# Kernel optimization log

Hardware: AMD Instinct MI355X
Metric: run time of the kernel (lower is better)

The kernel has to match this reference:

```python
import jax, jax.numpy as jnp
import numpy as np

B, N, I, H = 4, 325, 64, 128
LN_EPS = 1e-5

def setup_inputs() -> dict:
    key = jax.random.key(0)
    ks = jax.random.split(key, 20)
    x = jax.random.normal(ks[0], (B, N, I), dtype=jnp.float32)
    # sparse binary adjacency with self-loops (as the module masks adj == 0)
    a = (jax.random.uniform(ks[1], (B, N, N)) < 0.05).astype(jnp.float32)
    adj = jnp.maximum(a, jnp.eye(N, dtype=jnp.float32)[None])
    h = jax.random.normal(ks[2], (B, N, H), dtype=jnp.float32)
    c = jax.random.normal(ks[3], (B, N, H), dtype=jnp.float32)
    def glorot(k, shape):
        fan_in, fan_out = shape[-1], shape[0]
        s = jnp.sqrt(2.0 / (fan_in + fan_out)).astype(jnp.float32)
        return jax.random.normal(k, shape, dtype=jnp.float32) * s
    params = {
        'W_ih': glorot(ks[4], (4 * H, I)),
        'W_hh': glorot(ks[5], (4 * H, H)),
        'b_ih': jnp.zeros((4 * H,), jnp.float32),
        'b_hh': jnp.zeros((4 * H,), jnp.float32),
        'gc_w': glorot(ks[6], (H, H)),
        'gc_b': jnp.zeros((H,), jnp.float32),
        'Ws_w': glorot(ks[7], (H, H)),
        'Ws_b': jnp.zeros((H,), jnp.float32),
        'Wt_w': glorot(ks[8], (H, H)),
        'Wt_b': jnp.zeros((H,), jnp.float32),
        'v': glorot(ks[9], (H, 1)),
        'ln_g': jnp.ones((H,), jnp.float32),
        'ln_b': jnp.zeros((H,), jnp.float32),
        'comb_w': glorot(ks[10], (H, 2 * H)),
        'comb_b': jnp.zeros((H,), jnp.float32),
    }
    return {'x': x, 'adj': adj, 'h': h, 'c': c, **params}


def reference(x, adj, h, c, W_ih, W_hh, b_ih, b_hh, gc_w, gc_b,
              Ws_w, Ws_b, Wt_w, Wt_b, v, ln_g, ln_b, comb_w, comb_b):
    # --- LSTMCell applied per node (PyTorch gate order: i, f, g, o) ---
    gates = (jnp.einsum('bni,gi->bng', x, W_ih) + b_ih
             + jnp.einsum('bnh,gh->bng', h, W_hh) + b_hh)  # [B,N,4H]
    i_g, f_g, g_g, o_g = jnp.split(gates, 4, axis=-1)
    c_lstm = jax.nn.sigmoid(f_g) * c + jax.nn.sigmoid(i_g) * jnp.tanh(g_g)
    h_lstm = jax.nn.sigmoid(o_g) * jnp.tanh(c_lstm)  # [B,N,H]
    # --- Graph convolution: adj @ (h W) + b ---
    support = jnp.einsum('bnh,ho->bno', h_lstm, gc_w)
    h_graph = jnp.einsum('bnm,bmo->bno', adj, support) + gc_b
    # --- Spatial attention (tanh-additive, adjacency-masked softmax) ---
    s = jnp.einsum('bnh,oh->bno', h_graph, Ws_w) + Ws_b  # W_s(x)
    t = jnp.einsum('bnh,oh->bno', h_graph, Wt_w) + Wt_b  # W_t(x)
    # scores[b,i,j] = tanh(s[b,i] + t[b,j]) @ v ; big [B,N,N,H] intermediate
    scores = jnp.einsum('bijh,h->bij',
                        jnp.tanh(s[:, :, None, :] + t[:, None, :, :]),
                        v[:, 0])
    scores = jnp.where(adj == 0, -1e9, scores)
    attn = jax.nn.softmax(scores, axis=-1)
    context = jnp.einsum('bij,bjh->bih', attn, h_graph)
    # --- LayerNorm ---
    mu = jnp.mean(context, axis=-1, keepdims=True)
    var = jnp.var(context, axis=-1, keepdims=True)
    h_att = ln_g * (context - mu) * jax.lax.rsqrt(var + LN_EPS) + ln_b
    # --- Combine ---
    h_comb = jnp.concatenate([h_lstm, h_att], axis=-1)
    h_new = jnp.einsum('bnk,ok->bno', h_comb, comb_w) + comb_b
    return (h_new, c_lstm)
```

## Files before the change

### kernel.cpp

```cpp
#include <hip/hip_runtime.h>

#define B_ 4
#define N_ 325
#define I_ 64
#define H_ 128
#define NODES (B_ * N_)
#define NZMAX 64
#define NBLK (NODES / 4)

typedef unsigned short u16;
typedef unsigned int u32;

__device__ __align__(16) float g_WT   [192 * 512];
__device__ __align__(16) float g_gcw  [128 * 128];
__device__ __align__(16) float g_WsT  [128 * 128];
__device__ __align__(16) float g_WtT  [128 * 128];
__device__ __align__(16) float g_combT[256 * 128];
__device__ float g_bias[512];
__device__ float g_svec[896];

__device__ __align__(16) float g_support[(size_t)NODES * H_];
__device__ __align__(16) float g_h_graph[(size_t)NODES * H_];
__device__ __align__(16) float g_s_buf  [(size_t)NODES * H_];
__device__ __align__(16) float g_t_buf  [(size_t)NODES * H_];
__device__ __align__(16) float g_hl     [(size_t)NODES * H_];
__device__ u16 g_nz [(size_t)NODES * NZMAX];
__device__ int g_nzc[NODES];

__device__ __forceinline__ float bf2f(u16 u) { return __uint_as_float(((u32)u) << 16); }
__device__ __forceinline__ u16 f2bf(float f) {
    u32 u = __float_as_uint(f);
    u += 0x7fffu + ((u >> 16) & 1u);
    return (u16)(u >> 16);
}
__device__ __forceinline__ float ldin(const void* p, size_t i, int f32) {
    return f32 ? ((const float*)p)[i] : bf2f(((const u16*)p)[i]);
}
__device__ __forceinline__ void stout(void* p, size_t i, float v, int f32) {
    if (f32) ((float*)p)[i] = v; else ((u16*)p)[i] = f2bf(v);
}
__device__ __forceinline__ float fast_rcp(float x) { return __builtin_amdgcn_rcpf(x); }
__device__ __forceinline__ float sigm(float x) { return fast_rcp(1.f + __expf(-x)); }
__device__ __forceinline__ float tanh_f(float x) {
    x = fminf(15.f, fmaxf(-15.f, x));
    float e = __expf(2.f * x);
    return (e - 1.f) * fast_rcp(e + 1.f);
}
__device__ __forceinline__ int probe_f32(const void* adj) {
    return ((((const u32*)adj)[0] & 0xFFFFu) != 0x3F80u) ? 1 : 0;
}

__global__ __launch_bounds__(256) void k0_prep(
    const void* __restrict__ W_ih, const void* __restrict__ W_hh,
    const void* __restrict__ b_ih, const void* __restrict__ b_hh,
    const void* __restrict__ gc_w, const void* __restrict__ gc_b,
    const void* __restrict__ Ws_w, const void* __restrict__ Ws_b,
    const void* __restrict__ Wt_w, const void* __restrict__ Wt_b,
    const void* __restrict__ vvec, const void* __restrict__ ln_g,
    const void* __restrict__ ln_b, const void* __restrict__ comb_w,
    const void* __restrict__ comb_b, const void* __restrict__ adj)
{
    const int f32 = probe_f32(adj);
    const int tid = blockIdx.x * 256 + threadIdx.x;
    const int nth = gridDim.x * 256;
    const int TOT = 98304 + 16384 * 3 + 32768 + 512 + 896;
    for (int e = tid; e < TOT; e += nth) {
        int i = e;
        if (i < 98304) {
            const int k = i >> 9, g = i & 511;
            g_WT[i] = (k < 64) ? ldin(W_ih, (size_t)g * 64 + k, f32)
                               : ldin(W_hh, (size_t)g * 128 + (k - 64), f32);
            continue;
        }
        i -= 98304;
        if (i < 16384) { g_gcw[i] = ldin(gc_w, i, f32); continue; }
        i -= 16384;
        if (i < 16384) {
            const int k = i >> 7, o = i & 127;
            g_WsT[i] = ldin(Ws_w, (size_t)o * 128 + k, f32);
            continue;
        }
        i -= 16384;
        if (i < 16384) {
            const int k = i >> 7, o = i & 127;
            g_WtT[i] = ldin(Wt_w, (size_t)o * 128 + k, f32);
            continue;
        }
        i -= 16384;
        if (i < 32768) {
            const int k = i >> 7, o = i & 127;
            g_combT[i] = ldin(comb_w, (size_t)o * 256 + k, f32);
            continue;
        }
        i -= 32768;
        if (i < 512) { g_bias[i] = ldin(b_ih, i, f32) + ldin(b_hh, i, f32); continue; }
        i -= 512;
        {
            const int seg = i >> 7, k = i & 127;
            const void* src = (seg == 0) ? gc_b : (seg == 1) ? Ws_b : (seg == 2) ? Wt_b :
                              (seg == 3) ? vvec : (seg == 4) ? ln_g : (seg == 5) ? ln_b : comb_b;
            g_svec[i] = ldin(src, k, f32);
        }
    }
}

__global__ __launch_bounds__(512) void k1_lstm(
    const void* __restrict__ x, const void* __restrict__ h, const void* __restrict__ c,
    const void* __restrict__ adj, void* __restrict__ out)
{
    const int f32 = probe_f32(adj);
    __shared__ __align__(16) float4 xh4[192];
    __shared__ __align__(16) float4 Gt4[512];
    __shared__ __align__(16) float4 hl4[128];
    const int node0 = blockIdx.x * 4;
    const int t = threadIdx.x;

    for (int e = t; e < 768; e += 512) {
        const int n = e / 192, k = e % 192;
        const int node = node0 + n;
        ((float*)&xh4[k])[n] = (k < 64) ? ldin(x, (size_t)node * 64 + k, f32)
                                        : ldin(h, (size_t)node * 128 + (k - 64), f32);
    }
    __syncthreads();

    {
        const int g = t;
        float a0 = 0.f, a1 = 0.f, a2 = 0.f, a3 = 0.f;
        #pragma unroll 8
        for (int k = 0; k < 192; ++k) {
            const float wv = g_WT[(size_t)k * 512 + g];
            const float4 xv = xh4[k];
            a0 = fmaf(xv.x, wv, a0); a1 = fmaf(xv.y, wv, a1);
            a2 = fmaf(xv.z, wv, a2); a3 = fmaf(xv.w, wv, a3);
        }
        const float bias = g_bias[g];
        Gt4[g] = make_float4(a0 + bias, a1 + bias, a2 + bias, a3 + bias);
    }
    __syncthreads();

    {
        const int n = t >> 7, hh = t & 127;
        const int node = node0 + n;
        float ig = ((const float*)&Gt4[hh])[n];
        float fg = ((const float*)&Gt4[128 + hh])[n];
        float gv = ((const float*)&Gt4[256 + hh])[n];
        float og = ((const float*)&Gt4[384 + hh])[n];
        float cl = sigm(fg) * ldin(c, (size_t)node * 128 + hh, f32) + sigm(ig) * tanh_f(gv);
        float hv = sigm(og) * tanh_f(cl);
        stout(out, (size_t)(NODES * H_) + (size_t)node * 128 + hh, cl, f32);
        g_hl[(size_t)node * 128 + hh] = hv;
        ((float*)&hl4[hh])[n] = hv;
    }
    __syncthreads();

    {
        const int o = t & 127, n = t >> 7;
        float acc = 0.f;
        #pragma unroll 8
        for (int k = 0; k < 128; ++k)
            acc = fmaf(((const float*)&hl4[k])[n], g_gcw[(size_t)k * 128 + o], acc);
        g_support[(size_t)(node0 + n) * 128 + o] = acc;
    }
}

__global__ __launch_bounds__(256) void k2_graph(const void* __restrict__ adj)
{
    const int f32 = probe_f32(adj);
    __shared__ __align__(16) float4 hg4[128];
    __shared__ u16 nzi[4][NZMAX];
    __shared__ float nzv[4][NZMAX];
    __shared__ int cnt[4];
    const int node0 = blockIdx.x * 4;
    const int t = threadIdx.x;
    const int lane = t & 63, w = t >> 6;

    if (t < 4) cnt[t] = 0;
    __syncthreads();
    for (int j = lane; j < N_; j += 64) {
        float a = ldin(adj, (size_t)(node0 + w) * N_ + j, f32);
        if (a != 0.f) {
            int p = atomicAdd(&cnt[w], 1);
            if (p < NZMAX) { nzi[w][p] = (u16)j; nzv[w][p] = a; }
        }
    }
    __syncthreads();
    if (t < 4) g_nzc[node0 + t] = min(cnt[t], NZMAX);
    #pragma unroll
    for (int n = 0; n < 4; ++n) {
        const int cnn = min(cnt[n], NZMAX);
        for (int p = t; p < cnn; p += 256) g_nz[(size_t)(node0 + n) * NZMAX + p] = nzi[n][p];
    }

    const int o = t & 127;
    const float gb = g_svec[o];
    #pragma unroll
    for (int ps = 0; ps < 2; ++ps) {
        const int n = (t >> 7) + 2 * ps;
        const int node = node0 + n;
        const int bn = node / N_;
        const int cnn = min(cnt[n], NZMAX);
        float acc = gb;
        for (int p = 0; p < cnn; ++p)
            acc = fmaf(nzv[n][p], g_support[((size_t)bn * N_ + nzi[n][p]) * 128 + o], acc);
        g_h_graph[(size_t)node * 128 + o] = acc;
        ((float*)&hg4[o])[n] = acc;
    }
    __syncthreads();

    {
        const int which = t >> 7;
        const float* WT = which ? g_WtT : g_WsT;
        const float bias = g_svec[128 + which * 128 + o];
        float a0 = 0.f, a1 = 0.f, a2 = 0.f, a3 = 0.f;
        #pragma unroll 8
        for (int k = 0; k < 128; ++k) {
            const float wv = WT[(size_t)k * 128 + o];
            const float4 hv = hg4[k];
            a0 = fmaf(hv.x, wv, a0); a1 = fmaf(hv.y, wv, a1);
            a2 = fmaf(hv.z, wv, a2); a3 = fmaf(hv.w, wv, a3);
        }
        float* dst = which ? g_t_buf : g_s_buf;
        dst[(size_t)(node0 + 0) * 128 + o] = a0 + bias;
        dst[(size_t)(node0 + 1) * 128 + o] = a1 + bias;
        dst[(size_t)(node0 + 2) * 128 + o] = a2 + bias;
        dst[(size_t)(node0 + 3) * 128 + o] = a3 + bias;
    }
}

__global__ __launch_bounds__(256) void k3_attn(
    const void* __restrict__ adj, void* __restrict__ out)
{
    const int f32 = probe_f32(adj);
    __shared__ __align__(16) float4 comb4[256];
    __shared__ float s_i[4][H_];
    __shared__ float red[4][H_];
    __shared__ float nzs[4][NZMAX];
    __shared__ u16 nzi[4][NZMAX];
    __shared__ float part[2][4][H_];
    __shared__ float mu_[4], rstd_[4], smv[4];
    __shared__ int cnt[4];
    const int node0 = blockIdx.x * 4;
    const int t = threadIdx.x;
    const int lane = t & 63, w = t >> 6;

    if (t < 4) cnt[t] = g_nzc[node0 + t];
    for (int e = t; e < 512; e += 256) {
        const int n = e >> 7, k = e & 127;
        const int node = node0 + n;
        s_i[n][k] = g_s_buf[(size_t)node * 128 + k];
        ((float*)&comb4[k])[n] = g_hl[(size_t)node * 128 + k];
    }
    __syncthreads();
    #pragma unroll
    for (int n = 0; n < 4; ++n)
        for (int p = t; p < cnt[n]; p += 256) nzi[n][p] = g_nz[(size_t)(node0 + n) * NZMAX + p];
    __syncthreads();

    {
        const int bn = (node0 + w) / N_;
        const int cn = cnt[w];
        const float v0 = g_svec[384 + lane], v1 = g_svec[384 + 64 + lane];
        const float si0 = s_i[w][lane], si1 = s_i[w][lane + 64];
        for (int p = 0; p < cn; ++p) {
            const float* tj = g_t_buf + ((size_t)bn * N_ + nzi[w][p]) * 128;
            float a = v0 * tanh_f(si0 + tj[lane]) + v1 * tanh_f(si1 + tj[lane + 64]);
            #pragma unroll
            for (int off = 32; off > 0; off >>= 1) a += __shfl_xor(a, off);
            if (lane == 0) nzs[w][p] = a;
        }
    }
    __syncthreads();

    if (t < 4) {
        const int cn = cnt[t];
        float m = -1e30f;
        for (int p = 0; p < cn; ++p) m = fmaxf(m, nzs[t][p]);
        float ssum = 0.f;
        for (int p = 0; p < cn; ++p) { float e = __expf(nzs[t][p] - m); nzs[t][p] = e; ssum += e; }
        smv[t] = fast_rcp(ssum);
    }
    __syncthreads();

    const int o = t & 127;
    #pragma unroll
    for (int ps = 0; ps < 2; ++ps) {
        const int n = (t >> 7) + 2 * ps;
        const int bn = (node0 + n) / N_;
        const int cn = cnt[n];
        float acc = 0.f;
        for (int p = 0; p < cn; ++p)
            acc = fmaf(nzs[n][p], g_h_graph[((size_t)bn * N_ + nzi[n][p]) * 128 + o], acc);
        red[n][o] = acc * smv[n];
    }
    __syncthreads();

    {
        float x0 = red[w][lane], x1 = red[w][lane + 64];
        float sm = x0 + x1, sq = x0 * x0 + x1 * x1;
        #pragma unroll
        for (int off = 32; off > 0; off >>= 1) {
            sm += __shfl_xor(sm, off);
            sq += __shfl_xor(sq, off);
        }
        if (lane == 0) {
            float mu = sm * (1.f / H_);
            float var = fmaxf(sq * (1.f / H_) - mu * mu, 0.f);
            mu_[w] = mu;
            rstd_[w] = __builtin_amdgcn_rsqf(var + 1e-5f);
        }
    }
    __syncthreads();
    for (int e = t; e < 512; e += 256) {
        const int n = e >> 7, k = e & 127;
        float xn = (red[n][k] - mu_[n]) * rstd_[n];
        ((float*)&comb4[128 + k])[n] = g_svec[512 + k] * xn + g_svec[640 + k];
    }
    __syncthreads();

    {
        const int half = t >> 7;
        float a0 = 0.f, a1 = 0.f, a2 = 0.f, a3 = 0.f;
        const int k0 = half * 128;
        #pragma unroll 8
        for (int kk = 0; kk < 128; ++kk) {
            const int k = k0 + kk;
            const float wv = g_combT[(size_t)k * 128 + o];
            const float4 cv = comb4[k];
            a0 = fmaf(cv.x, wv, a0); a1 = fmaf(cv.y, wv, a1);
            a2 = fmaf(cv.z, wv, a2); a3 = fmaf(cv.w, wv, a3);
        }
        part[half][0][o] = a0; part[half][1][o] = a1;
        part[half][2][o] = a2; part[half][3][o] = a3;
    }
    __syncthreads();
    for (int e = t; e < 512; e += 256) {
        const int n = e >> 7, k = e & 127;
        stout(out, (size_t)(node0 + n) * 128 + k,
              part[0][n][k] + part[1][n][k] + g_svec[768 + k], f32);
    }
}

extern "C" void kernel_launch(void* const* d_in, const int* in_sizes, int n_in,
                              void* d_out, int out_size, void* d_ws, size_t ws_size,
                              hipStream_t stream)
{
    (void)in_sizes; (void)n_in; (void)out_size; (void)d_ws; (void)ws_size;
    const void* x      = d_in[0];
    const void* adj    = d_in[1];
    const void* h      = d_in[2];
    const void* c      = d_in[3];
    const void* W_ih   = d_in[4];
    const void* W_hh   = d_in[5];
    const void* b_ih   = d_in[6];
    const void* b_hh   = d_in[7];
    const void* gc_w   = d_in[8];
    const void* gc_b   = d_in[9];
    const void* Ws_w   = d_in[10];
    const void* Ws_b   = d_in[11];
    const void* Wt_w   = d_in[12];
    const void* Wt_b   = d_in[13];
    const void* vvec   = d_in[14];
    const void* ln_g   = d_in[15];
    const void* ln_b   = d_in[16];
    const void* comb_w = d_in[17];
    const void* comb_b = d_in[18];

    k0_prep <<<256, 256, 0, stream>>>(W_ih, W_hh, b_ih, b_hh, gc_w, gc_b,
                                      Ws_w, Ws_b, Wt_w, Wt_b, vvec, ln_g, ln_b,
                                      comb_w, comb_b, adj);
    k1_lstm <<<NBLK, 512, 0, stream>>>(x, h, c, adj, d_out);
    k2_graph<<<NBLK, 256, 0, stream>>>(adj);
    k3_attn <<<NBLK, 256, 0, stream>>>(adj, d_out);
}
```

Baseline: 152.2 us.

## Fuse prep, LSTM, graph and attention kernels into one cooperative kernel

```diff
diff --git a/kernel.cpp b/kernel.cpp
--- a/kernel.cpp
+++ b/kernel.cpp
@@ -1,4 +1,7 @@
 #include <hip/hip_runtime.h>
+#include <hip/hip_cooperative_groups.h>
+
+namespace cg = cooperative_groups;
 
 #define B_ 4
 #define N_ 325
@@ -21,8 +24,8 @@
 
 __device__ __align__(16) float g_support[(size_t)NODES * H_];
 __device__ __align__(16) float g_h_graph[(size_t)NODES * H_];
+__device__ __align__(16) float g_t_buf  [(size_t)NODES * H_];
 __device__ __align__(16) float g_s_buf  [(size_t)NODES * H_];
-__device__ __align__(16) float g_t_buf  [(size_t)NODES * H_];
 __device__ __align__(16) float g_hl     [(size_t)NODES * H_];
 __device__ u16 g_nz [(size_t)NODES * NZMAX];
 __device__ int g_nzc[NODES];
@@ -48,6 +51,273 @@
 }
 __device__ __forceinline__ int probe_f32(const void* adj) {
     return ((((const u32*)adj)[0] & 0xFFFFu) != 0x3F80u) ? 1 : 0;
+}
+
+#define PREP_TOT (98304 + 16384 * 3 + 32768 + 512 + 896)
+
+__device__ __forceinline__ void prep_elem(int e, int f32,
+    const void* W_ih, const void* W_hh, const void* b_ih, const void* b_hh,
+    const void* gc_w, const void* gc_b, const void* Ws_w, const void* Ws_b,
+    const void* Wt_w, const void* Wt_b, const void* vvec, const void* ln_g,
+    const void* ln_b, const void* comb_w, const void* comb_b)
+{
+    int i = e;
+    if (i < 98304) {
+        const int k = i >> 9, g = i & 511;
+        g_WT[i] = (k < 64) ? ldin(W_ih, (size_t)g * 64 + k, f32)
+                           : ldin(W_hh, (size_t)g * 128 + (k - 64), f32);
+        return;
+    }
+    i -= 98304;
+    if (i < 16384) { g_gcw[i] = ldin(gc_w, i, f32); return; }
+    i -= 16384;
+    if (i < 16384) {
+        const int k = i >> 7, o = i & 127;
+        g_WsT[i] = ldin(Ws_w, (size_t)o * 128 + k, f32);
+        return;
+    }
+    i -= 16384;
+    if (i < 16384) {
+        const int k = i >> 7, o = i & 127;
+        g_WtT[i] = ldin(Wt_w, (size_t)o * 128 + k, f32);
+        return;
+    }
+    i -= 16384;
+    if (i < 32768) {
+        const int k = i >> 7, o = i & 127;
+        g_combT[i] = ldin(comb_w, (size_t)o * 256 + k, f32);
+        return;
+    }
+    i -= 32768;
+    if (i < 512) { g_bias[i] = ldin(b_ih, i, f32) + ldin(b_hh, i, f32); return; }
+    i -= 512;
+    {
+        const int seg = i >> 7, k = i & 127;
+        const void* src = (seg == 0) ? gc_b : (seg == 1) ? Ws_b : (seg == 2) ? Wt_b :
+                          (seg == 3) ? vvec : (seg == 4) ? ln_g : (seg == 5) ? ln_b : comb_b;
+        g_svec[i] = ldin(src, k, f32);
+    }
+}
+
+__global__ __launch_bounds__(512, 4) void k_fused(
+    const void* __restrict__ x, const void* __restrict__ adj,
+    const void* __restrict__ h, const void* __restrict__ c,
+    const void* __restrict__ W_ih, const void* __restrict__ W_hh,
+    const void* __restrict__ b_ih, const void* __restrict__ b_hh,
+    const void* __restrict__ gc_w, const void* __restrict__ gc_b,
+    const void* __restrict__ Ws_w, const void* __restrict__ Ws_b,
+    const void* __restrict__ Wt_w, const void* __restrict__ Wt_b,
+    const void* __restrict__ vvec, const void* __restrict__ ln_g,
+    const void* __restrict__ ln_b, const void* __restrict__ comb_w,
+    const void* __restrict__ comb_b, void* __restrict__ out)
+{
+    cg::grid_group grid = cg::this_grid();
+    const int f32 = probe_f32(adj);
+    const int t = threadIdx.x;
+    const int node0 = blockIdx.x * 4;
+    const int lane = t & 63, w = t >> 6;
+
+    __shared__ __align__(16) float4 xh4[192];
+    __shared__ __align__(16) float4 Gt4[512];
+    __shared__ __align__(16) float4 hl4[128];
+    __shared__ __align__(16) float4 hg4[128];
+    __shared__ __align__(16) float4 att4[128];
+    __shared__ u16 nzi[4][NZMAX];
+    __shared__ float nzv[4][NZMAX];
+    __shared__ float nzs[4][NZMAX];
+    __shared__ int cnt[4];
+    __shared__ float s_i[4][H_];
+    __shared__ float red[4][H_];
+    __shared__ float part[4][4][H_];
+    __shared__ float mu_[4], rstd_[4], smv[4];
+
+    {
+        const int tid = blockIdx.x * 512 + t;
+        const int nth = gridDim.x * 512;
+        for (int e = tid; e < PREP_TOT; e += nth)
+            prep_elem(e, f32, W_ih, W_hh, b_ih, b_hh, gc_w, gc_b, Ws_w, Ws_b,
+                      Wt_w, Wt_b, vvec, ln_g, ln_b, comb_w, comb_b);
+    }
+    grid.sync();
+
+    for (int e = t; e < 768; e += 512) {
+        const int n = e / 192, k = e % 192;
+        const int node = node0 + n;
+        ((float*)&xh4[k])[n] = (k < 64) ? ldin(x, (size_t)node * 64 + k, f32)
+                                        : ldin(h, (size_t)node * 128 + (k - 64), f32);
+    }
+    __syncthreads();
+    {
+        const int g = t;
+        float a0 = 0.f, a1 = 0.f, a2 = 0.f, a3 = 0.f;
+        #pragma unroll 8
+        for (int k = 0; k < 192; ++k) {
+            const float wv = g_WT[(size_t)k * 512 + g];
+            const float4 xv = xh4[k];
+            a0 = fmaf(xv.x, wv, a0); a1 = fmaf(xv.y, wv, a1);
+            a2 = fmaf(xv.z, wv, a2); a3 = fmaf(xv.w, wv, a3);
+        }
+        const float bias = g_bias[g];
+        Gt4[g] = make_float4(a0 + bias, a1 + bias, a2 + bias, a3 + bias);
+    }
+    __syncthreads();
+    {
+        const int n = t >> 7, hh = t & 127;
+        const int node = node0 + n;
+        float ig = ((const float*)&Gt4[hh])[n];
+        float fg = ((const float*)&Gt4[128 + hh])[n];
+        float gv = ((const float*)&Gt4[256 + hh])[n];
+        float og = ((const float*)&Gt4[384 + hh])[n];
+        float cl = sigm(fg) * ldin(c, (size_t)node * 128 + hh, f32) + sigm(ig) * tanh_f(gv);
+        float hv = sigm(og) * tanh_f(cl);
+        stout(out, (size_t)(NODES * H_) + (size_t)node * 128 + hh, cl, f32);
+        ((float*)&hl4[hh])[n] = hv;
+    }
+    __syncthreads();
+    {
+        const int o = t & 127, n = t >> 7;
+        float acc = 0.f;
+        #pragma unroll 8
+        for (int k = 0; k < 128; ++k)
+            acc = fmaf(((const float*)&hl4[k])[n], g_gcw[(size_t)k * 128 + o], acc);
+        g_support[(size_t)(node0 + n) * 128 + o] = acc;
+    }
+    grid.sync();
+
+    if (t < 4) cnt[t] = 0;
+    __syncthreads();
+    {
+        const int n = t >> 7, jj = t & 127;
+        const size_t row = (size_t)(node0 + n) * N_;
+        for (int j = jj; j < N_; j += 128) {
+            float a = ldin(adj, row + j, f32);
+            if (a != 0.f) {
+                int p = atomicAdd(&cnt[n], 1);
+                if (p < NZMAX) { nzi[n][p] = (u16)j; nzv[n][p] = a; }
+            }
+        }
+    }
+    __syncthreads();
+    {
+        const int n = t >> 7, o = t & 127;
+        const int node = node0 + n;
+        const int bn = node / N_;
+        const int cn = min(cnt[n], NZMAX);
+        float acc = g_svec[o];
+        for (int p = 0; p < cn; ++p)
+            acc = fmaf(nzv[n][p], g_support[((size_t)bn * N_ + nzi[n][p]) * 128 + o], acc);
+        g_h_graph[(size_t)node * 128 + o] = acc;
+        ((float*)&hg4[o])[n] = acc;
+    }
+    __syncthreads();
+    {
+        const int o = t & 127;
+        const int which = (t >> 7) & 1;
+        const int half  = t >> 8;
+        const float* WT = which ? g_WtT : g_WsT;
+        const int k0 = half * 64;
+        float a0 = 0.f, a1 = 0.f, a2 = 0.f, a3 = 0.f;
+        #pragma unroll 8
+        for (int kk = 0; kk < 64; ++kk) {
+            const int k = k0 + kk;
+            const float wv = WT[(size_t)k * 128 + o];
+            const float4 hv = hg4[k];
+            a0 = fmaf(hv.x, wv, a0); a1 = fmaf(hv.y, wv, a1);
+            a2 = fmaf(hv.z, wv, a2); a3 = fmaf(hv.w, wv, a3);
+        }
+        const int s = which * 2 + half;
+        part[s][0][o] = a0; part[s][1][o] = a1;
+        part[s][2][o] = a2; part[s][3][o] = a3;
+    }
+    __syncthreads();
+    for (int e = t; e < 1024; e += 512) {
+        const int which = e >> 9, n = (e >> 7) & 3, o = e & 127;
+        const float vsum = part[which * 2][n][o] + part[which * 2 + 1][n][o]
+                         + g_svec[128 + which * 128 + o];
+        if (which) g_t_buf[(size_t)(node0 + n) * 128 + o] = vsum;
+        else       s_i[n][o] = vsum;
+    }
+    grid.sync();
+
+    {
+        const int n = w & 3;
+        const int bn = (node0 + n) / N_;
+        const int cn = min(cnt[n], NZMAX);
+        const float v0 = g_svec[384 + lane], v1 = g_svec[384 + 64 + lane];
+        const float si0 = s_i[n][lane], si1 = s_i[n][lane + 64];
+        for (int p = (w >> 2); p < cn; p += 2) {
+            const float* tj = g_t_buf + ((size_t)bn * N_ + nzi[n][p]) * 128;
+            float a = v0 * tanh_f(si0 + tj[lane]) + v1 * tanh_f(si1 + tj[lane + 64]);
+            #pragma unroll
+            for (int off = 32; off > 0; off >>= 1) a += __shfl_xor(a, off);
+            if (lane == 0) nzs[n][p] = a;
+        }
+    }
+    __syncthreads();
+    if (t < 4) {
+        const int cn = min(cnt[t], NZMAX);
+        float m = -1e30f;
+        for (int p = 0; p < cn; ++p) m = fmaxf(m, nzs[t][p]);
+        float ssum = 0.f;
+        for (int p = 0; p < cn; ++p) { float e = __expf(nzs[t][p] - m); nzs[t][p] = e; ssum += e; }
+        smv[t] = fast_rcp(ssum);
+    }
+    __syncthreads();
+    {
+        const int n = t >> 7, o = t & 127;
+        const int bn = (node0 + n) / N_;
+        const int cn = min(cnt[n], NZMAX);
+        float acc = 0.f;
+        for (int p = 0; p < cn; ++p)
+            acc = fmaf(nzs[n][p], g_h_graph[((size_t)bn * N_ + nzi[n][p]) * 128 + o], acc);
+        red[n][o] = acc * smv[n];
+    }
+    __syncthreads();
+    if (w < 4) {
+        float x0 = red[w][lane], x1 = red[w][lane + 64];
+        float sm = x0 + x1, sq = x0 * x0 + x1 * x1;
+        #pragma unroll
+        for (int off = 32; off > 0; off >>= 1) {
+            sm += __shfl_xor(sm, off);
+            sq += __shfl_xor(sq, off);
+        }
+        if (lane == 0) {
+            float mu = sm * (1.f / H_);
+            float var = fmaxf(sq * (1.f / H_) - mu * mu, 0.f);
+            mu_[w] = mu;
+            rstd_[w] = __builtin_amdgcn_rsqf(var + 1e-5f);
+        }
+    }
+    __syncthreads();
+    {
+        const int n = t >> 7, k = t & 127;
+        float xn = (red[n][k] - mu_[n]) * rstd_[n];
+        ((float*)&att4[k])[n] = g_svec[512 + k] * xn + g_svec[640 + k];
+    }
+    __syncthreads();
+    {
+        const int o = t & 127, q = t >> 7;
+        const float4* src = (q < 2) ? hl4 : att4;
+        const int kb = (q < 2) ? q * 64 : (q - 2) * 64;
+        const int k0 = q * 64;
+        float a0 = 0.f, a1 = 0.f, a2 = 0.f, a3 = 0.f;
+        #pragma unroll 8
+        for (int kk = 0; kk < 64; ++kk) {
+            const float wv = g_combT[(size_t)(k0 + kk) * 128 + o];
+            const float4 cv = src[kb + kk];
+            a0 = fmaf(cv.x, wv, a0); a1 = fmaf(cv.y, wv, a1);
+            a2 = fmaf(cv.z, wv, a2); a3 = fmaf(cv.w, wv, a3);
+        }
+        part[q][0][o] = a0; part[q][1][o] = a1;
+        part[q][2][o] = a2; part[q][3][o] = a3;
+    }
+    __syncthreads();
+    {
+        const int n = t >> 7, k = t & 127;
+        stout(out, (size_t)(node0 + n) * 128 + k,
+              part[0][n][k] + part[1][n][k] + part[2][n][k] + part[3][n][k]
+              + g_svec[768 + k], f32);
+    }
 }
 
 __global__ __launch_bounds__(256) void k0_prep(
@@ -63,45 +333,9 @@
     const int f32 = probe_f32(adj);
     const int tid = blockIdx.x * 256 + threadIdx.x;
     const int nth = gridDim.x * 256;
-    const int TOT = 98304 + 16384 * 3 + 32768 + 512 + 896;
-    for (int e = tid; e < TOT; e += nth) {
-        int i = e;
-        if (i < 98304) {
-            const int k = i >> 9, g = i & 511;
-            g_WT[i] = (k < 64) ? ldin(W_ih, (size_t)g * 64 + k, f32)
-                               : ldin(W_hh, (size_t)g * 128 + (k - 64), f32);
-            continue;
-        }
-        i -= 98304;
-        if (i < 16384) { g_gcw[i] = ldin(gc_w, i, f32); continue; }
-        i -= 16384;
-        if (i < 16384) {
-            const int k = i >> 7, o = i & 127;
-            g_WsT[i] = ldin(Ws_w, (size_t)o * 128 + k, f32);
-            continue;
-        }
-        i -= 16384;
-        if (i < 16384) {
-            const int k = i >> 7, o = i & 127;
-            g_WtT[i] = ldin(Wt_w, (size_t)o * 128 + k, f32);
-            continue;
-        }
-        i -= 16384;
-        if (i < 32768) {
-            const int k = i >> 7, o = i & 127;
-            g_combT[i] = ldin(comb_w, (size_t)o * 256 + k, f32);
-            continue;
-        }
-        i -= 32768;
-        if (i < 512) { g_bias[i] = ldin(b_ih, i, f32) + ldin(b_hh, i, f32); continue; }
-        i -= 512;
-        {
-            const int seg = i >> 7, k = i & 127;
-            const void* src = (seg == 0) ? gc_b : (seg == 1) ? Ws_b : (seg == 2) ? Wt_b :
-                              (seg == 3) ? vvec : (seg == 4) ? ln_g : (seg == 5) ? ln_b : comb_b;
-            g_svec[i] = ldin(src, k, f32);
-        }
-    }
+    for (int e = tid; e < PREP_TOT; e += nth)
+        prep_elem(e, f32, W_ih, W_hh, b_ih, b_hh, gc_w, gc_b, Ws_w, Ws_b,
+                  Wt_w, Wt_b, vvec, ln_g, ln_b, comb_w, comb_b);
 }
 
 __global__ __launch_bounds__(512) void k1_lstm(
@@ -122,7 +356,6 @@
                                         : ldin(h, (size_t)node * 128 + (k - 64), f32);
     }
     __syncthreads();
-
     {
         const int g = t;
         float a0 = 0.f, a1 = 0.f, a2 = 0.f, a3 = 0.f;
@@ -137,7 +370,6 @@
         Gt4[g] = make_float4(a0 + bias, a1 + bias, a2 + bias, a3 + bias);
     }
     __syncthreads();
-
     {
         const int n = t >> 7, hh = t & 127;
         const int node = node0 + n;
@@ -152,7 +384,6 @@
         ((float*)&hl4[hh])[n] = hv;
     }
     __syncthreads();
-
     {
         const int o = t & 127, n = t >> 7;
         float acc = 0.f;
@@ -206,7 +437,6 @@
         ((float*)&hg4[o])[n] = acc;
     }
     __syncthreads();
-
     {
         const int which = t >> 7;
         const float* WT = which ? g_WtT : g_WsT;
@@ -270,7 +500,6 @@
         }
     }
     __syncthreads();
-
     if (t < 4) {
         const int cn = cnt[t];
         float m = -1e30f;
@@ -280,7 +509,6 @@
         smv[t] = fast_rcp(ssum);
     }
     __syncthreads();
-
     const int o = t & 127;
     #pragma unroll
     for (int ps = 0; ps < 2; ++ps) {
@@ -293,7 +521,6 @@
         red[n][o] = acc * smv[n];
     }
     __syncthreads();
-
     {
         float x0 = red[w][lane], x1 = red[w][lane + 64];
         float sm = x0 + x1, sq = x0 * x0 + x1 * x1;
@@ -316,7 +543,6 @@
         ((float*)&comb4[128 + k])[n] = g_svec[512 + k] * xn + g_svec[640 + k];
     }
     __syncthreads();
-
     {
         const int half = t >> 7;
         float a0 = 0.f, a1 = 0.f, a2 = 0.f, a3 = 0.f;
@@ -365,10 +591,22 @@
     const void* comb_w = d_in[17];
     const void* comb_b = d_in[18];
 
-    k0_prep <<<256, 256, 0, stream>>>(W_ih, W_hh, b_ih, b_hh, gc_w, gc_b,
-                                      Ws_w, Ws_b, Wt_w, Wt_b, vvec, ln_g, ln_b,
-                                      comb_w, comb_b, adj);
-    k1_lstm <<<NBLK, 512, 0, stream>>>(x, h, c, adj, d_out);
-    k2_graph<<<NBLK, 256, 0, stream>>>(adj);
-    k3_attn <<<NBLK, 256, 0, stream>>>(adj, d_out);
-}
+    void* args[] = {
+        (void*)&x, (void*)&adj, (void*)&h, (void*)&c,
+        (void*)&W_ih, (void*)&W_hh, (void*)&b_ih, (void*)&b_hh,
+        (void*)&gc_w, (void*)&gc_b, (void*)&Ws_w, (void*)&Ws_b,
+        (void*)&Wt_w, (void*)&Wt_b, (void*)&vvec, (void*)&ln_g,
+        (void*)&ln_b, (void*)&comb_w, (void*)&comb_b, (void*)&d_out
+    };
+    hipError_t err = hipLaunchCooperativeKernel(
+        reinterpret_cast<void*>(k_fused), dim3(NBLK), dim3(512),
+        args, 0, stream);
+    if (err != hipSuccess) {
+        k0_prep <<<256, 256, 0, stream>>>(W_ih, W_hh, b_ih, b_hh, gc_w, gc_b,
+                                          Ws_w, Ws_b, Wt_w, Wt_b, vvec, ln_g, ln_b,
+                                          comb_w, comb_b, adj);
+        k1_lstm <<<NBLK, 512, 0, stream>>>(x, h, c, adj, d_out);
+        k2_graph<<<NBLK, 256, 0, stream>>>(adj);
+        k3_attn <<<NBLK, 256, 0, stream>>>(adj, d_out);
+    }
+}
```

Result: slower. 276.7 us (+81.9%).

## Drop weight-prep kernel, read raw weights directly, move adjacency compaction into LSTM kernel

Applied to the files above, without the earlier changes.

```diff
diff --git a/kernel.cpp b/kernel.cpp
--- a/kernel.cpp
+++ b/kernel.cpp
@@ -11,21 +11,14 @@
 typedef unsigned short u16;
 typedef unsigned int u32;
 
-__device__ __align__(16) float g_WT   [192 * 512];
-__device__ __align__(16) float g_gcw  [128 * 128];
-__device__ __align__(16) float g_WsT  [128 * 128];
-__device__ __align__(16) float g_WtT  [128 * 128];
-__device__ __align__(16) float g_combT[256 * 128];
-__device__ float g_bias[512];
-__device__ float g_svec[896];
-
 __device__ __align__(16) float g_support[(size_t)NODES * H_];
 __device__ __align__(16) float g_h_graph[(size_t)NODES * H_];
+__device__ __align__(16) float g_t_buf  [(size_t)NODES * H_];
 __device__ __align__(16) float g_s_buf  [(size_t)NODES * H_];
-__device__ __align__(16) float g_t_buf  [(size_t)NODES * H_];
 __device__ __align__(16) float g_hl     [(size_t)NODES * H_];
-__device__ u16 g_nz [(size_t)NODES * NZMAX];
-__device__ int g_nzc[NODES];
+__device__ u16   g_nz [(size_t)NODES * NZMAX];
+__device__ float g_nzw[(size_t)NODES * NZMAX];
+__device__ int   g_nzc[NODES];
 
 __device__ __forceinline__ float bf2f(u16 u) { return __uint_as_float(((u32)u) << 16); }
 __device__ __forceinline__ u16 f2bf(float f) {
@@ -33,11 +26,19 @@
     u += 0x7fffu + ((u >> 16) & 1u);
     return (u16)(u >> 16);
 }
-__device__ __forceinline__ float ldin(const void* p, size_t i, int f32) {
-    return f32 ? ((const float*)p)[i] : bf2f(((const u16*)p)[i]);
-}
-__device__ __forceinline__ void stout(void* p, size_t i, float v, int f32) {
-    if (f32) ((float*)p)[i] = v; else ((u16*)p)[i] = f2bf(v);
+template<int F32>
+__device__ __forceinline__ float ldw(const void* p, size_t i) {
+    return F32 ? ((const float*)p)[i] : bf2f(((const u16*)p)[i]);
+}
+template<int F32>
+__device__ __forceinline__ float4 ldw4(const void* p, size_t i4) {
+    if (F32) return ((const float4*)p)[i4];
+    const ushort4 u = ((const ushort4*)p)[i4];
+    return make_float4(bf2f(u.x), bf2f(u.y), bf2f(u.z), bf2f(u.w));
+}
+template<int F32>
+__device__ __forceinline__ void stw(void* p, size_t i, float v) {
+    if (F32) ((float*)p)[i] = v; else ((u16*)p)[i] = f2bf(v);
 }
 __device__ __forceinline__ float fast_rcp(float x) { return __builtin_amdgcn_rcpf(x); }
 __device__ __forceinline__ float sigm(float x) { return fast_rcp(1.f + __expf(-x)); }
@@ -50,174 +51,180 @@
     return ((((const u32*)adj)[0] & 0xFFFFu) != 0x3F80u) ? 1 : 0;
 }
 
-__global__ __launch_bounds__(256) void k0_prep(
+struct LdsA {
+    float4 xh4[192];
+    float4 Gt4[512];
+    float4 hl4[128];
+    u16 nzi[4][NZMAX];
+    float nzv[4][NZMAX];
+    int cnt[4];
+};
+
+template<int F32>
+__device__ __forceinline__ void d1_body(LdsA& S,
+    const void* __restrict__ x, const void* __restrict__ adjp,
+    const void* __restrict__ h, const void* __restrict__ c,
     const void* __restrict__ W_ih, const void* __restrict__ W_hh,
     const void* __restrict__ b_ih, const void* __restrict__ b_hh,
-    const void* __restrict__ gc_w, const void* __restrict__ gc_b,
-    const void* __restrict__ Ws_w, const void* __restrict__ Ws_b,
-    const void* __restrict__ Wt_w, const void* __restrict__ Wt_b,
-    const void* __restrict__ vvec, const void* __restrict__ ln_g,
-    const void* __restrict__ ln_b, const void* __restrict__ comb_w,
-    const void* __restrict__ comb_b, const void* __restrict__ adj)
-{
-    const int f32 = probe_f32(adj);
-    const int tid = blockIdx.x * 256 + threadIdx.x;
-    const int nth = gridDim.x * 256;
-    const int TOT = 98304 + 16384 * 3 + 32768 + 512 + 896;
-    for (int e = tid; e < TOT; e += nth) {
-        int i = e;
-        if (i < 98304) {
-            const int k = i >> 9, g = i & 511;
-            g_WT[i] = (k < 64) ? ldin(W_ih, (size_t)g * 64 + k, f32)
-                               : ldin(W_hh, (size_t)g * 128 + (k - 64), f32);
-            continue;
-        }
-        i -= 98304;
-        if (i < 16384) { g_gcw[i] = ldin(gc_w, i, f32); continue; }
-        i -= 16384;
-        if (i < 16384) {
-            const int k = i >> 7, o = i & 127;
-            g_WsT[i] = ldin(Ws_w, (size_t)o * 128 + k, f32);
-            continue;
-        }
-        i -= 16384;
-        if (i < 16384) {
-            const int k = i >> 7, o = i & 127;
-            g_WtT[i] = ldin(Wt_w, (size_t)o * 128 + k, f32);
-            continue;
-        }
-        i -= 16384;
-        if (i < 32768) {
-            const int k = i >> 7, o = i & 127;
-            g_combT[i] = ldin(comb_w, (size_t)o * 256 + k, f32);
-            continue;
-        }
-        i -= 32768;
-        if (i < 512) { g_bias[i] = ldin(b_ih, i, f32) + ldin(b_hh, i, f32); continue; }
-        i -= 512;
-        {
-            const int seg = i >> 7, k = i & 127;
-            const void* src = (seg == 0) ? gc_b : (seg == 1) ? Ws_b : (seg == 2) ? Wt_b :
-                              (seg == 3) ? vvec : (seg == 4) ? ln_g : (seg == 5) ? ln_b : comb_b;
-            g_svec[i] = ldin(src, k, f32);
-        }
-    }
-}
-
-__global__ __launch_bounds__(512) void k1_lstm(
-    const void* __restrict__ x, const void* __restrict__ h, const void* __restrict__ c,
-    const void* __restrict__ adj, void* __restrict__ out)
-{
-    const int f32 = probe_f32(adj);
-    __shared__ __align__(16) float4 xh4[192];
-    __shared__ __align__(16) float4 Gt4[512];
-    __shared__ __align__(16) float4 hl4[128];
+    const void* __restrict__ gc_w, void* __restrict__ out)
+{
+    const int t = threadIdx.x;
     const int node0 = blockIdx.x * 4;
-    const int t = threadIdx.x;
-
+
+    if (t < 4) S.cnt[t] = 0;
     for (int e = t; e < 768; e += 512) {
         const int n = e / 192, k = e % 192;
         const int node = node0 + n;
-        ((float*)&xh4[k])[n] = (k < 64) ? ldin(x, (size_t)node * 64 + k, f32)
-                                        : ldin(h, (size_t)node * 128 + (k - 64), f32);
+        ((float*)&S.xh4[k])[n] = (k < 64) ? ldw<F32>(x, (size_t)node * 64 + k)
+                                          : ldw<F32>(h, (size_t)node * 128 + (k - 64));
     }
     __syncthreads();
 
     {
         const int g = t;
         float a0 = 0.f, a1 = 0.f, a2 = 0.f, a3 = 0.f;
-        #pragma unroll 8
-        for (int k = 0; k < 192; ++k) {
-            const float wv = g_WT[(size_t)k * 512 + g];
-            const float4 xv = xh4[k];
-            a0 = fmaf(xv.x, wv, a0); a1 = fmaf(xv.y, wv, a1);
-            a2 = fmaf(xv.z, wv, a2); a3 = fmaf(xv.w, wv, a3);
-        }
-        const float bias = g_bias[g];
-        Gt4[g] = make_float4(a0 + bias, a1 + bias, a2 + bias, a3 + bias);
+        #pragma unroll 4
+        for (int k4 = 0; k4 < 16; ++k4) {
+            const float4 wv = ldw4<F32>(W_ih, (size_t)g * 16 + k4);
+            const float* wp = (const float*)&wv;
+            #pragma unroll
+            for (int j = 0; j < 4; ++j) {
+                const float4 xv = S.xh4[k4 * 4 + j];
+                a0 = fmaf(xv.x, wp[j], a0); a1 = fmaf(xv.y, wp[j], a1);
+                a2 = fmaf(xv.z, wp[j], a2); a3 = fmaf(xv.w, wp[j], a3);
+            }
+        }
+        #pragma unroll 4
+        for (int k4 = 0; k4 < 32; ++k4) {
+            const float4 wv = ldw4<F32>(W_hh, (size_t)g * 32 + k4);
+            const float* wp = (const float*)&wv;
+            #pragma unroll
+            for (int j = 0; j < 4; ++j) {
+                const float4 xv = S.xh4[64 + k4 * 4 + j];
+                a0 = fmaf(xv.x, wp[j], a0); a1 = fmaf(xv.y, wp[j], a1);
+                a2 = fmaf(xv.z, wp[j], a2); a3 = fmaf(xv.w, wp[j], a3);
+            }
+        }
+        const float bias = ldw<F32>(b_ih, t) + ldw<F32>(b_hh, t);
+        S.Gt4[g] = make_float4(a0 + bias, a1 + bias, a2 + bias, a3 + bias);
     }
     __syncthreads();
 
     {
         const int n = t >> 7, hh = t & 127;
         const int node = node0 + n;
-        float ig = ((const float*)&Gt4[hh])[n];
-        float fg = ((const float*)&Gt4[128 + hh])[n];
-        float gv = ((const float*)&Gt4[256 + hh])[n];
-        float og = ((const float*)&Gt4[384 + hh])[n];
-        float cl = sigm(fg) * ldin(c, (size_t)node * 128 + hh, f32) + sigm(ig) * tanh_f(gv);
+        float ig = ((const float*)&S.Gt4[hh])[n];
+        float fg = ((const float*)&S.Gt4[128 + hh])[n];
+        float gv = ((const float*)&S.Gt4[256 + hh])[n];
+        float og = ((const float*)&S.Gt4[384 + hh])[n];
+        float cl = sigm(fg) * ldw<F32>(c, (size_t)node * 128 + hh) + sigm(ig) * tanh_f(gv);
         float hv = sigm(og) * tanh_f(cl);
-        stout(out, (size_t)(NODES * H_) + (size_t)node * 128 + hh, cl, f32);
+        stw<F32>(out, (size_t)(NODES * H_) + (size_t)node * 128 + hh, cl);
         g_hl[(size_t)node * 128 + hh] = hv;
-        ((float*)&hl4[hh])[n] = hv;
-    }
-    __syncthreads();
-
+        ((float*)&S.hl4[hh])[n] = hv;
+    }
+    {
+        const int n = t >> 7, jj = t & 127;
+        const size_t row = (size_t)(node0 + n) * N_;
+        for (int j = jj; j < N_; j += 128) {
+            float a = ldw<F32>(adjp, row + j);
+            if (a != 0.f) {
+                int p = atomicAdd(&S.cnt[n], 1);
+                if (p < NZMAX) { S.nzi[n][p] = (u16)j; S.nzv[n][p] = a; }
+            }
+        }
+    }
+    __syncthreads();
+
+    if (t < 4) g_nzc[node0 + t] = min(S.cnt[t], NZMAX);
+    #pragma unroll
+    for (int n = 0; n < 4; ++n) {
+        const int cnn = min(S.cnt[n], NZMAX);
+        for (int p = t; p < cnn; p += 512) {
+            g_nz [(size_t)(node0 + n) * NZMAX + p] = S.nzi[n][p];
+            g_nzw[(size_t)(node0 + n) * NZMAX + p] = S.nzv[n][p];
+        }
+    }
     {
         const int o = t & 127, n = t >> 7;
         float acc = 0.f;
         #pragma unroll 8
         for (int k = 0; k < 128; ++k)
-            acc = fmaf(((const float*)&hl4[k])[n], g_gcw[(size_t)k * 128 + o], acc);
+            acc = fmaf(((const float*)&S.hl4[k])[n], ldw<F32>(gc_w, (size_t)k * 128 + o), acc);
         g_support[(size_t)(node0 + n) * 128 + o] = acc;
     }
 }
 
-__global__ __launch_bounds__(256) void k2_graph(const void* __restrict__ adj)
-{
-    const int f32 = probe_f32(adj);
-    __shared__ __align__(16) float4 hg4[128];
-    __shared__ u16 nzi[4][NZMAX];
-    __shared__ float nzv[4][NZMAX];
-    __shared__ int cnt[4];
+__global__ __launch_bounds__(512) void kd1(
+    const void* __restrict__ x, const void* __restrict__ adj,
+    const void* __restrict__ h, const void* __restrict__ c,
+    const void* __restrict__ W_ih, const void* __restrict__ W_hh,
+    const void* __restrict__ b_ih, const void* __restrict__ b_hh,
+    const void* __restrict__ gc_w, void* __restrict__ out)
+{
+    __shared__ LdsA S;
+    if (probe_f32(adj)) d1_body<1>(S, x, adj, h, c, W_ih, W_hh, b_ih, b_hh, gc_w, out);
+    else                d1_body<0>(S, x, adj, h, c, W_ih, W_hh, b_ih, b_hh, gc_w, out);
+}
+
+struct LdsB {
+    float4 hg4[128];
+    u16 nzi[4][NZMAX];
+    float nzv[4][NZMAX];
+    int cnt[4];
+};
+
+template<int F32>
+__device__ __forceinline__ void d2_body(LdsB& S,
+    const void* __restrict__ gc_b, const void* __restrict__ Ws_w,
+    const void* __restrict__ Ws_b, const void* __restrict__ Wt_w,
+    const void* __restrict__ Wt_b)
+{
+    const int t = threadIdx.x;
     const int node0 = blockIdx.x * 4;
-    const int t = threadIdx.x;
-    const int lane = t & 63, w = t >> 6;
-
-    if (t < 4) cnt[t] = 0;
-    __syncthreads();
-    for (int j = lane; j < N_; j += 64) {
-        float a = ldin(adj, (size_t)(node0 + w) * N_ + j, f32);
-        if (a != 0.f) {
-            int p = atomicAdd(&cnt[w], 1);
-            if (p < NZMAX) { nzi[w][p] = (u16)j; nzv[w][p] = a; }
-        }
-    }
-    __syncthreads();
-    if (t < 4) g_nzc[node0 + t] = min(cnt[t], NZMAX);
+
+    if (t < 4) S.cnt[t] = g_nzc[node0 + t];
+    __syncthreads();
     #pragma unroll
     for (int n = 0; n < 4; ++n) {
-        const int cnn = min(cnt[n], NZMAX);
-        for (int p = t; p < cnn; p += 256) g_nz[(size_t)(node0 + n) * NZMAX + p] = nzi[n][p];
-    }
+        const int cnn = S.cnt[n];
+        for (int p = t; p < cnn; p += 256) {
+            S.nzi[n][p] = g_nz [(size_t)(node0 + n) * NZMAX + p];
+            S.nzv[n][p] = g_nzw[(size_t)(node0 + n) * NZMAX + p];
+        }
+    }
+    __syncthreads();
 
     const int o = t & 127;
-    const float gb = g_svec[o];
     #pragma unroll
     for (int ps = 0; ps < 2; ++ps) {
         const int n = (t >> 7) + 2 * ps;
         const int node = node0 + n;
         const int bn = node / N_;
-        const int cnn = min(cnt[n], NZMAX);
-        float acc = gb;
+        const int cnn = S.cnt[n];
+        float acc = ldw<F32>(gc_b, o);
         for (int p = 0; p < cnn; ++p)
-            acc = fmaf(nzv[n][p], g_support[((size_t)bn * N_ + nzi[n][p]) * 128 + o], acc);
+            acc = fmaf(S.nzv[n][p], g_support[((size_t)bn * N_ + S.nzi[n][p]) * 128 + o], acc);
         g_h_graph[(size_t)node * 128 + o] = acc;
-        ((float*)&hg4[o])[n] = acc;
+        ((float*)&S.hg4[o])[n] = acc;
     }
     __syncthreads();
 
     {
         const int which = t >> 7;
-        const float* WT = which ? g_WtT : g_WsT;
-        const float bias = g_svec[128 + which * 128 + o];
+        const void* W = which ? Wt_w : Ws_w;
+        const float bias = ldw<F32>(which ? Wt_b : Ws_b, o);
         float a0 = 0.f, a1 = 0.f, a2 = 0.f, a3 = 0.f;
-        #pragma unroll 8
-        for (int k = 0; k < 128; ++k) {
-            const float wv = WT[(size_t)k * 128 + o];
-            const float4 hv = hg4[k];
-            a0 = fmaf(hv.x, wv, a0); a1 = fmaf(hv.y, wv, a1);
-            a2 = fmaf(hv.z, wv, a2); a3 = fmaf(hv.w, wv, a3);
+        #pragma unroll 4
+        for (int k4 = 0; k4 < 32; ++k4) {
+            const float4 wv = ldw4<F32>(W, (size_t)o * 32 + k4);
+            const float* wp = (const float*)&wv;
+            #pragma unroll
+            for (int j = 0; j < 4; ++j) {
+                const float4 hv = S.hg4[k4 * 4 + j];
+                a0 = fmaf(hv.x, wp[j], a0); a1 = fmaf(hv.y, wp[j], a1);
+                a2 = fmaf(hv.z, wp[j], a2); a3 = fmaf(hv.w, wp[j], a3);
+            }
         }
         float* dst = which ? g_t_buf : g_s_buf;
         dst[(size_t)(node0 + 0) * 128 + o] = a0 + bias;
@@ -227,57 +234,72 @@
     }
 }
 
-__global__ __launch_bounds__(256) void k3_attn(
-    const void* __restrict__ adj, void* __restrict__ out)
-{
-    const int f32 = probe_f32(adj);
-    __shared__ __align__(16) float4 comb4[256];
-    __shared__ float s_i[4][H_];
-    __shared__ float red[4][H_];
-    __shared__ float nzs[4][NZMAX];
-    __shared__ u16 nzi[4][NZMAX];
-    __shared__ float part[2][4][H_];
-    __shared__ float mu_[4], rstd_[4], smv[4];
-    __shared__ int cnt[4];
+__global__ __launch_bounds__(256) void kd2(
+    const void* __restrict__ adj, const void* __restrict__ gc_b,
+    const void* __restrict__ Ws_w, const void* __restrict__ Ws_b,
+    const void* __restrict__ Wt_w, const void* __restrict__ Wt_b)
+{
+    __shared__ LdsB S;
+    if (probe_f32(adj)) d2_body<1>(S, gc_b, Ws_w, Ws_b, Wt_w, Wt_b);
+    else                d2_body<0>(S, gc_b, Ws_w, Ws_b, Wt_w, Wt_b);
+}
+
+struct LdsC {
+    float4 comb4[256];
+    float s_i[4][H_];
+    float red[4][H_];
+    float nzs[4][NZMAX];
+    u16 nzi[4][NZMAX];
+    float part[2][4][H_];
+    float mu_[4], rstd_[4], smv[4];
+    int cnt[4];
+};
+
+template<int F32>
+__device__ __forceinline__ void d3_body(LdsC& S,
+    const void* __restrict__ vvec, const void* __restrict__ ln_g,
+    const void* __restrict__ ln_b, const void* __restrict__ comb_w,
+    const void* __restrict__ comb_b, void* __restrict__ out)
+{
+    const int t = threadIdx.x;
     const int node0 = blockIdx.x * 4;
-    const int t = threadIdx.x;
     const int lane = t & 63, w = t >> 6;
 
-    if (t < 4) cnt[t] = g_nzc[node0 + t];
+    if (t < 4) S.cnt[t] = g_nzc[node0 + t];
     for (int e = t; e < 512; e += 256) {
         const int n = e >> 7, k = e & 127;
         const int node = node0 + n;
-        s_i[n][k] = g_s_buf[(size_t)node * 128 + k];
-        ((float*)&comb4[k])[n] = g_hl[(size_t)node * 128 + k];
+        S.s_i[n][k] = g_s_buf[(size_t)node * 128 + k];
+        ((float*)&S.comb4[k])[n] = g_hl[(size_t)node * 128 + k];
     }
     __syncthreads();
     #pragma unroll
     for (int n = 0; n < 4; ++n)
-        for (int p = t; p < cnt[n]; p += 256) nzi[n][p] = g_nz[(size_t)(node0 + n) * NZMAX + p];
+        for (int p = t; p < S.cnt[n]; p += 256)
+            S.nzi[n][p] = g_nz[(size_t)(node0 + n) * NZMAX + p];
     __syncthreads();
 
     {
         const int bn = (node0 + w) / N_;
-        const int cn = cnt[w];
-        const float v0 = g_svec[384 + lane], v1 = g_svec[384 + 64 + lane];
-        const float si0 = s_i[w][lane], si1 = s_i[w][lane + 64];
+        const int cn = S.cnt[w];
+        const float v0 = ldw<F32>(vvec, lane), v1 = ldw<F32>(vvec, 64 + lane);
+        const float si0 = S.s_i[w][lane], si1 = S.s_i[w][lane + 64];
         for (int p = 0; p < cn; ++p) {
-            const float* tj = g_t_buf + ((size_t)bn * N_ + nzi[w][p]) * 128;
+            const float* tj = g_t_buf + ((size_t)bn * N_ + S.nzi[w][p]) * 128;
             float a = v0 * tanh_f(si0 + tj[lane]) + v1 * tanh_f(si1 + tj[lane + 64]);
             #pragma unroll
             for (int off = 32; off > 0; off >>= 1) a += __shfl_xor(a, off);
-            if (lane == 0) nzs[w][p] = a;
-        }
-    }
-    __syncthreads();
-
+            if (lane == 0) S.nzs[w][p] = a;
+        }
+    }
+    __syncthreads();
     if (t < 4) {
-        const int cn = cnt[t];
+        const int cn = S.cnt[t];
         float m = -1e30f;
-        for (int p = 0; p < cn; ++p) m = fmaxf(m, nzs[t][p]);
+        for (int p = 0; p < cn; ++p) m = fmaxf(m, S.nzs[t][p]);
         float ssum = 0.f;
-        for (int p = 0; p < cn; ++p) { float e = __expf(nzs[t][p] - m); nzs[t][p] = e; ssum += e; }
-        smv[t] = fast_rcp(ssum);
+        for (int p = 0; p < cn; ++p) { float e = __expf(S.nzs[t][p] - m); S.nzs[t][p] = e; ssum += e; }
+        S.smv[t] = fast_rcp(ssum);
     }
     __syncthreads();
 
@@ -286,16 +308,16 @@
     for (int ps = 0; ps < 2; ++ps) {
         const int n = (t >> 7) + 2 * ps;
         const int bn = (node0 + n) / N_;
-        const int cn = cnt[n];
+        const int cn = S.cnt[n];
         float acc = 0.f;
         for (int p = 0; p < cn; ++p)
-            acc = fmaf(nzs[n][p], g_h_graph[((size_t)bn * N_ + nzi[n][p]) * 128 + o], acc);
-        red[n][o] = acc * smv[n];
-    }
-    __syncthreads();
-
-    {
-        float x0 = red[w][lane], x1 = red[w][lane + 64];
+            acc = fmaf(S.nzs[n][p], g_h_graph[((size_t)bn * N_ + S.nzi[n][p]) * 128 + o], acc);
+        S.red[n][o] = acc * S.smv[n];
+    }
+    __syncthreads();
+
+    {
+        float x0 = S.red[w][lane], x1 = S.red[w][lane + 64];
         float sm = x0 + x1, sq = x0 * x0 + x1 * x1;
         #pragma unroll
         for (int off = 32; off > 0; off >>= 1) {
@@ -305,39 +327,52 @@
         if (lane == 0) {
             float mu = sm * (1.f / H_);
             float var = fmaxf(sq * (1.f / H_) - mu * mu, 0.f);
-            mu_[w] = mu;
-            rstd_[w] = __builtin_amdgcn_rsqf(var + 1e-5f);
+            S.mu_[w] = mu;
+            S.rstd_[w] = __builtin_amdgcn_rsqf(var + 1e-5f);
         }
     }
     __syncthreads();
     for (int e = t; e < 512; e += 256) {
         const int n = e >> 7, k = e & 127;
-        float xn = (red[n][k] - mu_[n]) * rstd_[n];
-        ((float*)&comb4[128 + k])[n] = g_svec[512 + k] * xn + g_svec[640 + k];
+        float xn = (S.red[n][k] - S.mu_[n]) * S.rstd_[n];
+        ((float*)&S.comb4[128 + k])[n] = ldw<F32>(ln_g, k) * xn + ldw<F32>(ln_b, k);
     }
     __syncthreads();
 
     {
         const int half = t >> 7;
         float a0 = 0.f, a1 = 0.f, a2 = 0.f, a3 = 0.f;
-        const int k0 = half * 128;
-        #pragma unroll 8
-        for (int kk = 0; kk < 128; ++kk) {
-            const int k = k0 + kk;
-            const float wv = g_combT[(size_t)k * 128 + o];
-            const float4 cv = comb4[k];
-            a0 = fmaf(cv.x, wv, a0); a1 = fmaf(cv.y, wv, a1);
-            a2 = fmaf(cv.z, wv, a2); a3 = fmaf(cv.w, wv, a3);
-        }
-        part[half][0][o] = a0; part[half][1][o] = a1;
-        part[half][2][o] = a2; part[half][3][o] = a3;
+        #pragma unroll 4
+        for (int k4 = 0; k4 < 32; ++k4) {
+            const float4 wv = ldw4<F32>(comb_w, (size_t)o * 64 + half * 32 + k4);
+            const float* wp = (const float*)&wv;
+            #pragma unroll
+            for (int j = 0; j < 4; ++j) {
+                const float4 cv = S.comb4[half * 128 + k4 * 4 + j];
+                a0 = fmaf(cv.x, wp[j], a0); a1 = fmaf(cv.y, wp[j], a1);
+                a2 = fmaf(cv.z, wp[j], a2); a3 = fmaf(cv.w, wp[j], a3);
+            }
+        }
+        S.part[half][0][o] = a0; S.part[half][1][o] = a1;
+        S.part[half][2][o] = a2; S.part[half][3][o] = a3;
     }
     __syncthreads();
     for (int e = t; e < 512; e += 256) {
         const int n = e >> 7, k = e & 127;
-        stout(out, (size_t)(node0 + n) * 128 + k,
-              part[0][n][k] + part[1][n][k] + g_svec[768 + k], f32);
-    }
+        stw<F32>(out, (size_t)(node0 + n) * 128 + k,
+                 S.part[0][n][k] + S.part[1][n][k] + ldw<F32>(comb_b, k));
+    }
+}
+
+__global__ __launch_bounds__(256) void kd3(
+    const void* __restrict__ adj, const void* __restrict__ vvec,
+    const void* __restrict__ ln_g, const void* __restrict__ ln_b,
+    const void* __restrict__ comb_w, const void* __restrict__ comb_b,
+    void* __restrict__ out)
+{
+    __shared__ LdsC S;
+    if (probe_f32(adj)) d3_body<1>(S, vvec, ln_g, ln_b, comb_w, comb_b, out);
+    else                d3_body<0>(S, vvec, ln_g, ln_b, comb_w, comb_b, out);
 }
 
 extern "C" void kernel_launch(void* const* d_in, const int* in_sizes, int n_in,
@@ -365,10 +400,7 @@
     const void* comb_w = d_in[17];
     const void* comb_b = d_in[18];
 
-    k0_prep <<<256, 256, 0, stream>>>(W_ih, W_hh, b_ih, b_hh, gc_w, gc_b,
-                                      Ws_w, Ws_b, Wt_w, Wt_b, vvec, ln_g, ln_b,
-                                      comb_w, comb_b, adj);
-    k1_lstm <<<NBLK, 512, 0, stream>>>(x, h, c, adj, d_out);
-    k2_graph<<<NBLK, 256, 0, stream>>>(adj);
-    k3_attn <<<NBLK, 256, 0, stream>>>(adj, d_out);
-}
+    kd1<<<NBLK, 512, 0, stream>>>(x, adj, h, c, W_ih, W_hh, b_ih, b_hh, gc_w, d_out);
+    kd2<<<NBLK, 256, 0, stream>>>(adj, gc_b, Ws_w, Ws_b, Wt_w, Wt_b);
+    kd3<<<NBLK, 256, 0, stream>>>(adj, vvec, ln_g, ln_b, comb_w, comb_b, d_out);
+}
```

New measurement: 162.8 us. 7.0% more time.
